# Kernel optimization log

Hardware: AMD Instinct MI355X
Metric: run time of the kernel (lower is better)

## Reference

```python
import jax, jax.numpy as jnp
import numpy as np

DIMS = [1024, 2048, 1024, 1024]


def setup_inputs() -> dict:
    key = jax.random.key(0)
    ks = jax.random.split(key, 13)
    d_in, h1, h2, d_out = DIMS
    s = lambda k, shape, fan_in: jax.random.normal(k, shape, dtype=jnp.float32) / np.sqrt(fan_in)
    return {
        "x": jax.random.normal(ks[0], (4, 2048, d_in), dtype=jnp.float32),
        "w1": s(ks[1], (h1, d_in), d_in), "b1": jnp.zeros((h1,), jnp.float32),
        "w2": s(ks[2], (h2, h1), h1), "b2": jnp.zeros((h2,), jnp.float32),
        "wq": s(ks[3], (h2, h2), h2), "bq": jnp.zeros((h2,), jnp.float32),
        "wk": s(ks[4], (h2, h2), h2), "bk": jnp.zeros((h2,), jnp.float32),
        "wv": s(ks[5], (h2, h2), h2), "bv": jnp.zeros((h2,), jnp.float32),
        "wo": s(ks[6], (d_out, h2), h2), "bo": jnp.zeros((d_out,), jnp.float32),
    }


def reference(x, w1, b1, w2, b2, wq, bq, wk, bk, wv, bv, wo, bo):
    # MLP: Linear + ReLU twice (torch Linear: x @ W^T + b)
    h = jax.nn.relu(jnp.einsum('bsd,hd->bsh', x, w1) + b1)
    h = jax.nn.relu(jnp.einsum('bsh,eh->bse', h, w2) + b2)
    # Self-attention (single head over full hidden_dim)
    q = jnp.einsum('bse,fe->bsf', h, wq) + bq
    k = jnp.einsum('bse,fe->bsf', h, wk) + bk
    v = jnp.einsum('bse,fe->bsf', h, wv) + bv
    hidden_dim = wq.shape[0]
    scores = jnp.einsum('bsf,btf->bst', q, k) / jnp.sqrt(jnp.float32(hidden_dim))
    attn = jax.nn.softmax(scores, axis=-1)
    ctx = jnp.einsum('bst,btf->bsf', attn, v) + v  # residual with V
    return jnp.einsum('bsf,of->bso', ctx, wo) + bo
```

## Files before the change

### kernel.cpp

```cpp
#include <hip/hip_runtime.h>
#include <hip/hip_bf16.h>

typedef __bf16 bf16;
typedef bf16 bf16x8 __attribute__((ext_vector_type(8)));
typedef float f32x4 __attribute__((ext_vector_type(4)));

#define EPI_BIAS_RELU  0
#define EPI_BIAS_BF16  1
#define EPI_PLAIN_BF16 2
#define EPI_RESID      3
#define EPI_BIAS_F32   4

__device__ __forceinline__ void lds_load16(const bf16* g, bf16* l) {
  __builtin_amdgcn_global_load_lds((__attribute__((address_space(1))) void*)g,
                                   (__attribute__((address_space(3))) void*)l,
                                   16, 0, 0);
}

template<int N> __device__ __forceinline__ void vmw() {
  if constexpr (N == 0) asm volatile("s_waitcnt vmcnt(0)" ::: "memory");
  else if constexpr (N == 2) asm volatile("s_waitcnt vmcnt(2)" ::: "memory");
  else if constexpr (N == 4) asm volatile("s_waitcnt vmcnt(4)" ::: "memory");
}
__device__ __forceinline__ void barrier() { asm volatile("s_barrier" ::: "memory"); }

__device__ __forceinline__ void xcd_map(int& bx, int& by, int& z) {
  const int gx = gridDim.x, gy = gridDim.y;
  const int Y8 = (gy * gridDim.z) >> 3;
  const int L = (blockIdx.z * gy + blockIdx.y) * gx + blockIdx.x;
  const int xcd = L & 7, j = L >> 3;
  bx = j % gx;
  const int yy = xcd * Y8 + j / gx;
  by = yy % gy;
  z  = yy / gy;
}

template<int EPI>
__global__ __launch_bounds__(512, 2)
void gemm2x(const bf16* __restrict__ A, const bf16* __restrict__ B,
            void* __restrict__ Cv, const float* __restrict__ bias,
            int K, int lda, int ldb, int ldc,
            long long sAz, long long sBz, long long sCz)
{
  constexpr int BK = 64;
  constexpr int M_REP = 8, N_REP = 4, NH = 2;

  __shared__ __align__(16) bf16 lA[2][256 * BK];
  __shared__ __align__(16) bf16 lB[2][256 * BK];

  int bx, by, z;
  xcd_map(bx, by, z);

  const bf16* Ab = A + (size_t)z * sAz;
  const bf16* Bb = B + (size_t)z * sBz;
  const int row0 = by * 256, col0 = bx * 256;
  const int tid = threadIdx.x, w = tid >> 6, l = tid & 63;
  const int wr = w >> 2, wc = w & 3;

  const int srow = l >> 3, scb = (l & 7) ^ srow;
  const bf16* gA = Ab + (size_t)(row0 + w * 8 + srow) * lda + scb * 8;
  const bf16* gB = Bb + (size_t)(col0 + w * 8 + srow) * ldb + scb * 8;

  auto issueA = [&](int buf, int k0) {
#pragma unroll
    for (int i = 0; i < 4; i++)
      lds_load16(gA + (size_t)(i * 64) * lda + k0,
                 &lA[buf][(i * 64 + w * 8) * BK]);
  };
  auto issueB = [&](int buf, int k0) {
#pragma unroll
    for (int i = 0; i < 4; i++)
      lds_load16(gB + (size_t)(i * 64) * ldb + k0,
                 &lB[buf][(i * 64 + w * 8) * BK]);
  };

  const int fr = l & 15, fq = l >> 4, sw = fr & 7;
  bf16x8 aA[M_REP][2], bB0[NH][2], bB1[NH][2];
  f32x4 acc[M_REP][N_REP] = {};

  auto readAfull = [&](int buf) {
#pragma unroll
    for (int m = 0; m < M_REP; m++) {
      const int r = (m >> 2) * 128 + wr * 64 + (m & 3) * 16 + fr;
      const bf16* base = &lA[buf][r * BK];
#pragma unroll
      for (int kk = 0; kk < 2; kk++)
        aA[m][kk] = *(const bf16x8*)(base + ((kk * 4 + fq) ^ sw) * 8);
    }
  };
  auto readB = [&](bf16x8 (&dst)[NH][2], int buf, int h) {
#pragma unroll
    for (int nn = 0; nn < NH; nn++) {
      const bf16* base = &lB[buf][(h * 128 + wc * 32 + nn * 16 + fr) * BK];
#pragma unroll
      for (int kk = 0; kk < 2; kk++)
        dst[nn][kk] = *(const bf16x8*)(base + ((kk * 4 + fq) ^ sw) * 8);
    }
  };
  auto quad32 = [&](const bf16x8 (&b)[NH][2], int nBase) {
    __builtin_amdgcn_s_setprio(1);
#pragma unroll
    for (int m = 0; m < M_REP; m++)
#pragma unroll
      for (int nh = 0; nh < NH; nh++)
#pragma unroll
        for (int kk = 0; kk < 2; kk++)
          acc[m][nBase + nh] = __builtin_amdgcn_mfma_f32_16x16x32_bf16(
              aA[m][kk], b[nh][kk], acc[m][nBase + nh], 0, 0, 0);
    __builtin_amdgcn_s_setprio(0);
  };

  const int NT = K / BK;
  issueA(0, 0); issueB(0, 0); issueA(1, BK);
  vmw<4>();
  barrier();

  for (int t = 0; t < NT; t++) {
    const int cur = t & 1, nxt = cur ^ 1;
    const bool s1 = (t + 1 < NT), s2 = (t + 2 < NT);
    readAfull(cur);
    readB(bB0, cur, 0);
    if (s1) issueB(nxt, (t + 1) * BK);
    barrier();
    quad32(bB0, 0);
    barrier();
    readB(bB1, cur, 1);
    if (s2) { issueA(cur, (t + 2) * BK); vmw<4>(); }
    else vmw<0>();
    barrier();
    quad32(bB1, NH);
    barrier();
  }

#pragma unroll
  for (int m = 0; m < M_REP; m++) {
#pragma unroll
    for (int n = 0; n < N_REP; n++) {
      const int col = col0 + (n / NH) * 128 + wc * 32 + (n % NH) * 16 + fr;
#pragma unroll
      for (int j = 0; j < 4; j++) {
        const int rrow = row0 + (m >> 2) * 128 + wr * 64 + (m & 3) * 16 + fq * 4 + j;
        const float val = acc[m][n][j];
        if constexpr (EPI == EPI_PLAIN_BF16) {
          bf16* Cp = (bf16*)Cv + (size_t)z * sCz;
          Cp[(size_t)rrow * ldc + col] = (bf16)val;
        } else if constexpr (EPI == EPI_BIAS_BF16) {
          bf16* Cp = (bf16*)Cv;
          Cp[(size_t)rrow * ldc + col] = (bf16)(val + bias[col]);
        } else if constexpr (EPI == EPI_BIAS_RELU) {
          bf16* Cp = (bf16*)Cv;
          Cp[(size_t)rrow * ldc + col] = (bf16)fmaxf(val + bias[col], 0.f);
        }
      }
    }
  }
}

template<int EPI>
__global__ __launch_bounds__(512, 2)
void gemm2p(const bf16* __restrict__ A, const bf16* __restrict__ B,
            void* __restrict__ Cv, const float* __restrict__ bias,
            const bf16* __restrict__ resid,
            int K, int lda, int ldb, int ldc, int ldr,
            long long sAz, long long sBz, long long sCz, long long sRz)
{
  constexpr int BM = 128, BK = 64;
  constexpr int M_REP = 4, NH = 2;

  __shared__ __align__(16) bf16 lA[2][BM * BK];
  __shared__ __align__(16) bf16 lB[2][256 * BK];

  int bx, by, z;
  xcd_map(bx, by, z);

  const bf16* Ab = A + (size_t)z * sAz;
  const bf16* Bb = B + (size_t)z * sBz;
  const int row0 = by * BM, col0 = bx * 256;
  const int tid = threadIdx.x, w = tid >> 6, l = tid & 63;
  const int wr = w >> 2, wc = w & 3;

  const int srow = l >> 3, scb = (l & 7) ^ srow;
  const bf16* gA = Ab + (size_t)(row0 + w * 8 + srow) * lda + scb * 8;
  const bf16* gB = Bb + (size_t)(col0 + w * 8 + srow) * ldb + scb * 8;

  auto issueAfull = [&](int buf, int k0) {
#pragma unroll
    for (int i = 0; i < 2; i++)
      lds_load16(gA + (size_t)(i * 64) * lda + k0,
                 &lA[buf][(i * 64 + w * 8) * BK]);
  };
  auto issueBfull = [&](int buf, int k0) {
#pragma unroll
    for (int i = 0; i < 4; i++)
      lds_load16(gB + (size_t)(i * 64) * ldb + k0,
                 &lB[buf][(i * 64 + w * 8) * BK]);
  };

  const int fr = l & 15, fq = l >> 4, sw = fr & 7;
  bf16x8 aA[M_REP][2], bB0[NH][2], bB1[NH][2];
  f32x4 acc[M_REP][4] = {};

  auto readAfull = [&](int buf) {
#pragma unroll
    for (int m = 0; m < M_REP; m++) {
      const bf16* base = &lA[buf][(wr * 64 + m * 16 + fr) * BK];
#pragma unroll
      for (int kk = 0; kk < 2; kk++)
        aA[m][kk] = *(const bf16x8*)(base + ((kk * 4 + fq) ^ sw) * 8);
    }
  };
  auto readB = [&](bf16x8 (&dst)[NH][2], int buf, int h) {
#pragma unroll
    for (int nn = 0; nn < NH; nn++) {
      const bf16* base = &lB[buf][(h * 128 + wc * 32 + nn * 16 + fr) * BK];
#pragma unroll
      for (int kk = 0; kk < 2; kk++)
        dst[nn][kk] = *(const bf16x8*)(base + ((kk * 4 + fq) ^ sw) * 8);
    }
  };
  auto quad2 = [&](const bf16x8 (&b)[NH][2], int nBase) {
    __builtin_amdgcn_s_setprio(1);
#pragma unroll
    for (int m = 0; m < M_REP; m++)
#pragma unroll
      for (int nh = 0; nh < NH; nh++)
#pragma unroll
        for (int kk = 0; kk < 2; kk++)
          acc[m][nBase + nh] = __builtin_amdgcn_mfma_f32_16x16x32_bf16(
              aA[m][kk], b[nh][kk], acc[m][nBase + nh], 0, 0, 0);
    __builtin_amdgcn_s_setprio(0);
  };

  const int NT = K / BK;
  issueAfull(0, 0); issueBfull(0, 0); issueAfull(1, BK);
  vmw<2>();
  barrier();

  for (int t = 0; t < NT; t++) {
    const int cur = t & 1, nxt = cur ^ 1;
    const bool s1 = (t + 1 < NT), s2 = (t + 2 < NT);
    readAfull(cur);
    readB(bB0, cur, 0);
    if (s1) issueBfull(nxt, (t + 1) * BK);
    barrier();
    quad2(bB0, 0);
    barrier();
    readB(bB1, cur, 1);
    if (s2) { issueAfull(cur, (t + 2) * BK); vmw<2>(); }
    else vmw<0>();
    barrier();
    quad2(bB1, NH);
    barrier();
  }

#pragma unroll
  for (int m = 0; m < M_REP; m++) {
#pragma unroll
    for (int n = 0; n < 4; n++) {
      const int col = col0 + (n / NH) * 128 + wc * 32 + (n % NH) * 16 + fr;
#pragma unroll
      for (int j = 0; j < 4; j++) {
        const int rrow = row0 + wr * 64 + m * 16 + fq * 4 + j;
        const float val = acc[m][n][j];
        if constexpr (EPI == EPI_PLAIN_BF16) {
          bf16* Cp = (bf16*)Cv + (size_t)z * sCz;
          Cp[(size_t)rrow * ldc + col] = (bf16)val;
        } else if constexpr (EPI == EPI_BIAS_F32) {
          float* Cp = (float*)Cv;
          Cp[(size_t)rrow * ldc + col] = val + bias[col];
        } else if constexpr (EPI == EPI_BIAS_BF16) {
          bf16* Cp = (bf16*)Cv;
          Cp[(size_t)rrow * ldc + col] = (bf16)(val + bias[col]);
        } else if constexpr (EPI == EPI_BIAS_RELU) {
          bf16* Cp = (bf16*)Cv;
          Cp[(size_t)rrow * ldc + col] = (bf16)fmaxf(val + bias[col], 0.f);
        } else {
          bf16* Cp = (bf16*)Cv + (size_t)z * sCz;
          const bf16* Rp = resid + (size_t)z * sRz;
          Cp[(size_t)rrow * ldc + col] = (bf16)(val + (float)Rp[(size_t)rrow * ldr + col]);
        }
      }
    }
  }
}

__global__ __launch_bounds__(256)
void cast_all(const float* __restrict__ x,  const float* __restrict__ w1,
              const float* __restrict__ w2, const float* __restrict__ wq,
              const float* __restrict__ wk, const float* __restrict__ wv,
              const float* __restrict__ wo,
              bf16* __restrict__ xb, bf16* __restrict__ w1b,
              bf16* __restrict__ w2b, bf16* __restrict__ wqkb,
              bf16* __restrict__ wvb, bf16* __restrict__ wob) {
  const int b = blockIdx.x;
  const float* src; bf16* dst; int base; float scale = 1.f;
  if (b < 4096)      { src = x;  dst = xb;   base = b; }
  else if (b < 5120) { src = w1; dst = w1b;  base = b - 4096; }
  else if (b < 6144) { src = w2; dst = w2b;  base = b - 5120; }
  else if (b < 6656) { src = wq; dst = wqkb;              base = b - 6144; scale = 0.03125f; }
  else if (b < 7168) { src = wk; dst = wqkb + (1 << 20);  base = b - 6656; }
  else if (b < 7680) { src = wv; dst = wvb;  base = b - 7168; }
  else               { src = wo; dst = wob;  base = b - 7680; }
  const int i = base * 256 + threadIdx.x;
  const float4* p = (const float4*)src;
  float4 a = p[2 * i], c = p[2 * i + 1];
  bf16x8 o8;
  o8[0] = (bf16)(a.x * scale); o8[1] = (bf16)(a.y * scale);
  o8[2] = (bf16)(a.z * scale); o8[3] = (bf16)(a.w * scale);
  o8[4] = (bf16)(c.x * scale); o8[5] = (bf16)(c.y * scale);
  o8[6] = (bf16)(c.z * scale); o8[7] = (bf16)(c.w * scale);
  ((bf16x8*)dst)[i] = o8;
}

__global__ __launch_bounds__(256)
void pack_bias_qk(const float* __restrict__ bq, const float* __restrict__ bk,
                  float* __restrict__ o) {
  int i = blockIdx.x * 256 + threadIdx.x;
  o[i] = (i < 1024) ? bq[i] * 0.03125f : bk[i - 1024];
}

__global__ __launch_bounds__(256)
void transpose_bf16(const bf16* __restrict__ in, bf16* __restrict__ out,
                    int R, int C, int ldi,
                    long long inZ, long long outZ) {
  __shared__ bf16 t[64][72];
  const bf16* ib = in + (size_t)blockIdx.z * inZ;
  bf16* ob = out + (size_t)blockIdx.z * outZ;
  const int r0 = blockIdx.y * 64, c0 = blockIdx.x * 64;
  const int tid = threadIdx.x;
#pragma unroll
  for (int p = 0; p < 2; p++) {
    int r = p * 32 + tid / 8, cc = (tid % 8) * 8;
    bf16x8 vv = *(const bf16x8*)(ib + (size_t)(r0 + r) * ldi + c0 + cc);
#pragma unroll
    for (int j = 0; j < 8; j++) t[r][cc + j] = vv[j];
  }
  __syncthreads();
#pragma unroll
  for (int p = 0; p < 2; p++) {
    int r = p * 32 + tid / 8, cc = (tid % 8) * 8;
    bf16x8 o;
#pragma unroll
    for (int j = 0; j < 8; j++) o[j] = t[cc + j][r];
    *(bf16x8*)(ob + (size_t)(c0 + r) * R + r0 + cc) = o;
  }
}

__global__ __launch_bounds__(256)
void softmax_rows(bf16* __restrict__ S) {
  const size_t row = blockIdx.x;
  const int t = threadIdx.x, wv_ = t >> 6, ln = t & 63;
  bf16x8 v8 = ((const bf16x8*)(S + row * 2048))[t];
  float v[8];
#pragma unroll
  for (int j = 0; j < 8; j++) v[j] = (float)v8[j];
  float m = v[0];
#pragma unroll
  for (int j = 1; j < 8; j++) m = fmaxf(m, v[j]);
  for (int o = 32; o; o >>= 1) m = fmaxf(m, __shfl_xor(m, o));
  __shared__ float redm[4], reds[4];
  if (ln == 0) redm[wv_] = m;
  __syncthreads();
  m = fmaxf(fmaxf(redm[0], redm[1]), fmaxf(redm[2], redm[3]));
  float e[8], s = 0.f;
#pragma unroll
  for (int j = 0; j < 8; j++) { e[j] = __expf(v[j] - m); s += e[j]; }
  for (int o = 32; o; o >>= 1) s += __shfl_xor(s, o);
  if (ln == 0) reds[wv_] = s;
  __syncthreads();
  s = reds[0] + reds[1] + reds[2] + reds[3];
  const float inv = 1.f / s;
  bf16x8 o8;
#pragma unroll
  for (int j = 0; j < 8; j++) o8[j] = (bf16)(e[j] * inv);
  ((bf16x8*)(S + row * 2048))[t] = o8;
}

extern "C" void kernel_launch(void* const* d_in, const int* in_sizes, int n_in,
                              void* d_out, int out_size, void* d_ws, size_t ws_size,
                              hipStream_t stream) {
  const float* x  = (const float*)d_in[0];
  const float* w1 = (const float*)d_in[1];
  const float* b1 = (const float*)d_in[2];
  const float* w2 = (const float*)d_in[3];
  const float* b2 = (const float*)d_in[4];
  const float* wq = (const float*)d_in[5];
  const float* bq = (const float*)d_in[6];
  const float* wk = (const float*)d_in[7];
  const float* bk = (const float*)d_in[8];
  const float* wv = (const float*)d_in[9];
  const float* bv = (const float*)d_in[10];
  const float* wo = (const float*)d_in[11];
  const float* bo = (const float*)d_in[12];
  float* out = (float*)d_out;

  char* ws = (char*)d_ws;
  const size_t MB = 1024ull * 1024ull;
  if (ws_size < 130 * MB) return;

  bf16* w1b  = (bf16*)(ws + 0 * MB);
  bf16* w2b  = (bf16*)(ws + 4 * MB);
  bf16* wqkb = (bf16*)(ws + 8 * MB);
  bf16* wvb  = (bf16*)(ws + 12 * MB);
  bf16* wob  = (bf16*)(ws + 14 * MB);
  float* bqk = (float*)(ws + 16 * MB);
  bf16* xb  = (bf16*)(ws + 17 * MB);
  bf16* h1  = (bf16*)(ws + 33 * MB);
  bf16* h   = (bf16*)(ws + 65 * MB);
  bf16* qk  = (bf16*)(ws + 81 * MB);
  bf16* vb  = (bf16*)(ws + 113 * MB);
  bf16* vT  = (bf16*)(ws + 17 * MB);
  bf16* S   = (bf16*)(ws + 33 * MB);
  bf16* ctx = (bf16*)(ws + 65 * MB);

  cast_all<<<8192, 256, 0, stream>>>(x, w1, w2, wq, wk, wv, wo,
                                     xb, w1b, w2b, wqkb, wvb, wob);
  pack_bias_qk<<<8, 256, 0, stream>>>(bq, bk, bqk);

  gemm2x<EPI_BIAS_RELU><<<dim3(8, 32, 1), 512, 0, stream>>>(
      xb, w1b, h1, b1, 1024, 1024, 1024, 2048, 0, 0, 0);
  gemm2p<EPI_BIAS_RELU><<<dim3(4, 64, 1), 512, 0, stream>>>(
      h1, w2b, h, b2, nullptr, 2048, 2048, 2048, 1024, 0, 0, 0, 0, 0);
  gemm2x<EPI_BIAS_BF16><<<dim3(8, 32, 1), 512, 0, stream>>>(
      h, wqkb, qk, bqk, 1024, 1024, 1024, 2048, 0, 0, 0);
  gemm2p<EPI_BIAS_BF16><<<dim3(4, 64, 1), 512, 0, stream>>>(
      h, wvb, vb, bv, nullptr, 1024, 1024, 1024, 1024, 0, 0, 0, 0, 0);
  transpose_bf16<<<dim3(16, 32, 4), 256, 0, stream>>>(
      vb, vT, 2048, 1024, 1024, 2048LL * 1024, 1024LL * 2048);
  gemm2x<EPI_PLAIN_BF16><<<dim3(8, 8, 4), 512, 0, stream>>>(
      qk, qk + 1024, S, nullptr, 1024, 2048, 2048, 2048,
      2048LL * 2048, 2048LL * 2048, 2048LL * 2048);
  softmax_rows<<<8192, 256, 0, stream>>>(S);
  gemm2p<EPI_RESID><<<dim3(4, 16, 4), 512, 0, stream>>>(
      S, vT, ctx, nullptr, vb, 2048, 2048, 2048, 1024, 1024,
      2048LL * 2048, 1024LL * 2048, 2048LL * 1024, 2048LL * 1024);
  gemm2p<EPI_BIAS_F32><<<dim3(4, 64, 1), 512, 0, stream>>>(
      ctx, wob, out, bo, nullptr, 1024, 1024, 1024, 1024, 0, 0, 0, 0, 0);
}
```

Before: 266.6 us.

## Fuse fp32-to-bf16 cast of x into first GEMM and merge bias packing

Adds a gemm2xa kernel that loads fp32 x directly from global memory into registers, converts it to bf16 and writes it to LDS, so the separate cast pass over x and its bf16 copy in the workspace are no longer needed. The weight cast kernel also absorbs the q/k bias packing, which removes one launch. MFMA loop order in the existing GEMMs is changed to iterate kk outermost. In exchange, the first GEMM reads A at twice the bytes and performs the register-staged conversion inside the main loop, which adds VGPR pressure and manual vmcnt/lgkmcnt waits.

```diff
diff --git a/kernel.cpp b/kernel.cpp
--- a/kernel.cpp
+++ b/kernel.cpp
@@ -21,6 +21,10 @@
   if constexpr (N == 0) asm volatile("s_waitcnt vmcnt(0)" ::: "memory");
   else if constexpr (N == 2) asm volatile("s_waitcnt vmcnt(2)" ::: "memory");
   else if constexpr (N == 4) asm volatile("s_waitcnt vmcnt(4)" ::: "memory");
+  else if constexpr (N == 8) asm volatile("s_waitcnt vmcnt(8)" ::: "memory");
+}
+__device__ __forceinline__ void lgkm0() {
+  asm volatile("s_waitcnt lgkmcnt(0)" ::: "memory");
 }
 __device__ __forceinline__ void barrier() { asm volatile("s_barrier" ::: "memory"); }
 
@@ -100,11 +104,11 @@
   auto quad32 = [&](const bf16x8 (&b)[NH][2], int nBase) {
     __builtin_amdgcn_s_setprio(1);
 #pragma unroll
-    for (int m = 0; m < M_REP; m++)
-#pragma unroll
-      for (int nh = 0; nh < NH; nh++)
-#pragma unroll
-        for (int kk = 0; kk < 2; kk++)
+    for (int kk = 0; kk < 2; kk++)
+#pragma unroll
+      for (int m = 0; m < M_REP; m++)
+#pragma unroll
+        for (int nh = 0; nh < NH; nh++)
           acc[m][nBase + nh] = __builtin_amdgcn_mfma_f32_16x16x32_bf16(
               aA[m][kk], b[nh][kk], acc[m][nBase + nh], 0, 0, 0);
     __builtin_amdgcn_s_setprio(0);
@@ -156,6 +160,140 @@
   }
 }
 
+__global__ __launch_bounds__(512, 2)
+void gemm2xa(const float* __restrict__ Af, const bf16* __restrict__ B,
+             bf16* __restrict__ C, const float* __restrict__ bias,
+             int K, int lda, int ldb, int ldc)
+{
+  constexpr int BK = 64;
+  constexpr int M_REP = 8, N_REP = 4, NH = 2;
+
+  __shared__ __align__(16) bf16 lA[2][256 * BK];
+  __shared__ __align__(16) bf16 lB[2][256 * BK];
+
+  int bx, by, z;
+  xcd_map(bx, by, z);
+
+  const int row0 = by * 256, col0 = bx * 256;
+  const int tid = threadIdx.x, w = tid >> 6, l = tid & 63;
+  const int wr = w >> 2, wc = w & 3;
+
+  const int srow = l >> 3, cb0 = l & 7, scb = cb0 ^ srow;
+  const float* gAf = Af + (size_t)(row0 + w * 8 + srow) * lda + cb0 * 8;
+  const bf16*  gB  = B  + (size_t)(col0 + w * 8 + srow) * ldb + scb * 8;
+
+  float4 aST[4][2];
+
+  auto loadA = [&](int k0) {
+#pragma unroll
+    for (int i = 0; i < 4; i++) {
+      const float* p = gAf + (size_t)(i * 64) * lda + k0;
+      aST[i][0] = *(const float4*)(p);
+      aST[i][1] = *(const float4*)(p + 4);
+    }
+  };
+  auto writeA = [&](int buf) {
+#pragma unroll
+    for (int i = 0; i < 4; i++) {
+      bf16x8 o;
+      o[0] = (bf16)aST[i][0].x; o[1] = (bf16)aST[i][0].y;
+      o[2] = (bf16)aST[i][0].z; o[3] = (bf16)aST[i][0].w;
+      o[4] = (bf16)aST[i][1].x; o[5] = (bf16)aST[i][1].y;
+      o[6] = (bf16)aST[i][1].z; o[7] = (bf16)aST[i][1].w;
+      *(bf16x8*)(&lA[buf][(i * 64 + w * 8 + srow) * BK + scb * 8]) = o;
+    }
+  };
+  auto issueB = [&](int buf, int k0) {
+#pragma unroll
+    for (int i = 0; i < 4; i++)
+      lds_load16(gB + (size_t)(i * 64) * ldb + k0,
+                 &lB[buf][(i * 64 + w * 8) * BK]);
+  };
+
+  const int fr = l & 15, fq = l >> 4, sw = fr & 7;
+  bf16x8 aA[M_REP][2], bB0[NH][2], bB1[NH][2];
+  f32x4 acc[M_REP][N_REP] = {};
+
+  auto readAfull = [&](int buf) {
+#pragma unroll
+    for (int m = 0; m < M_REP; m++) {
+      const int r = (m >> 2) * 128 + wr * 64 + (m & 3) * 16 + fr;
+      const bf16* base = &lA[buf][r * BK];
+#pragma unroll
+      for (int kk = 0; kk < 2; kk++)
+        aA[m][kk] = *(const bf16x8*)(base + ((kk * 4 + fq) ^ sw) * 8);
+    }
+  };
+  auto readB = [&](bf16x8 (&dst)[NH][2], int buf, int h) {
+#pragma unroll
+    for (int nn = 0; nn < NH; nn++) {
+      const bf16* base = &lB[buf][(h * 128 + wc * 32 + nn * 16 + fr) * BK];
+#pragma unroll
+      for (int kk = 0; kk < 2; kk++)
+        dst[nn][kk] = *(const bf16x8*)(base + ((kk * 4 + fq) ^ sw) * 8);
+    }
+  };
+  auto quad32 = [&](const bf16x8 (&b)[NH][2], int nBase) {
+    __builtin_amdgcn_s_setprio(1);
+#pragma unroll
+    for (int kk = 0; kk < 2; kk++)
+#pragma unroll
+      for (int m = 0; m < M_REP; m++)
+#pragma unroll
+        for (int nh = 0; nh < NH; nh++)
+          acc[m][nBase + nh] = __builtin_amdgcn_mfma_f32_16x16x32_bf16(
+              aA[m][kk], b[nh][kk], acc[m][nBase + nh], 0, 0, 0);
+    __builtin_amdgcn_s_setprio(0);
+  };
+
+  const int NT = K / BK;
+  loadA(0);
+  issueB(0, 0);
+  vmw<4>();
+  writeA(0);
+  loadA(BK);
+  vmw<8>();
+  lgkm0();
+  barrier();
+
+  for (int t = 0; t < NT; t++) {
+    const int cur = t & 1, nxt = cur ^ 1;
+    const bool s1 = (t + 1 < NT), s2 = (t + 2 < NT);
+    readAfull(cur);
+    readB(bB0, cur, 0);
+    if (s1) issueB(nxt, (t + 1) * BK);
+    barrier();
+    quad32(bB0, 0);
+    barrier();
+    readB(bB1, cur, 1);
+    if (s1) {
+      vmw<4>();
+      writeA(nxt);
+      if (s2) { loadA((t + 2) * BK); vmw<8>(); }
+      else vmw<0>();
+      lgkm0();
+    } else {
+      vmw<0>();
+    }
+    barrier();
+    quad32(bB1, NH);
+    barrier();
+  }
+
+#pragma unroll
+  for (int m = 0; m < M_REP; m++) {
+#pragma unroll
+    for (int n = 0; n < N_REP; n++) {
+      const int col = col0 + (n / NH) * 128 + wc * 32 + (n % NH) * 16 + fr;
+#pragma unroll
+      for (int j = 0; j < 4; j++) {
+        const int rrow = row0 + (m >> 2) * 128 + wr * 64 + (m & 3) * 16 + fq * 4 + j;
+        C[(size_t)rrow * ldc + col] = (bf16)fmaxf(acc[m][n][j] + bias[col], 0.f);
+      }
+    }
+  }
+}
+
 template<int EPI>
 __global__ __launch_bounds__(512, 2)
 void gemm2p(const bf16* __restrict__ A, const bf16* __restrict__ B,
@@ -221,11 +359,11 @@
   auto quad2 = [&](const bf16x8 (&b)[NH][2], int nBase) {
     __builtin_amdgcn_s_setprio(1);
 #pragma unroll
-    for (int m = 0; m < M_REP; m++)
-#pragma unroll
-      for (int nh = 0; nh < NH; nh++)
-#pragma unroll
-        for (int kk = 0; kk < 2; kk++)
+    for (int kk = 0; kk < 2; kk++)
+#pragma unroll
+      for (int m = 0; m < M_REP; m++)
+#pragma unroll
+        for (int nh = 0; nh < NH; nh++)
           acc[m][nBase + nh] = __builtin_amdgcn_mfma_f32_16x16x32_bf16(
               aA[m][kk], b[nh][kk], acc[m][nBase + nh], 0, 0, 0);
     __builtin_amdgcn_s_setprio(0);
@@ -285,22 +423,26 @@
 }
 
 __global__ __launch_bounds__(256)
-void cast_all(const float* __restrict__ x,  const float* __restrict__ w1,
-              const float* __restrict__ w2, const float* __restrict__ wq,
-              const float* __restrict__ wk, const float* __restrict__ wv,
-              const float* __restrict__ wo,
-              bf16* __restrict__ xb, bf16* __restrict__ w1b,
-              bf16* __restrict__ w2b, bf16* __restrict__ wqkb,
-              bf16* __restrict__ wvb, bf16* __restrict__ wob) {
+void cast_w(const float* __restrict__ w1, const float* __restrict__ w2,
+            const float* __restrict__ wq, const float* __restrict__ wk,
+            const float* __restrict__ wv, const float* __restrict__ wo,
+            const float* __restrict__ bq, const float* __restrict__ bk,
+            bf16* __restrict__ w1b, bf16* __restrict__ w2b,
+            bf16* __restrict__ wqkb, bf16* __restrict__ wvb,
+            bf16* __restrict__ wob, float* __restrict__ bqk) {
   const int b = blockIdx.x;
+  if (b >= 4096) {
+    const int i = (b - 4096) * 256 + threadIdx.x;
+    bqk[i] = (i < 1024) ? bq[i] * 0.03125f : bk[i - 1024];
+    return;
+  }
   const float* src; bf16* dst; int base; float scale = 1.f;
-  if (b < 4096)      { src = x;  dst = xb;   base = b; }
-  else if (b < 5120) { src = w1; dst = w1b;  base = b - 4096; }
-  else if (b < 6144) { src = w2; dst = w2b;  base = b - 5120; }
-  else if (b < 6656) { src = wq; dst = wqkb;              base = b - 6144; scale = 0.03125f; }
-  else if (b < 7168) { src = wk; dst = wqkb + (1 << 20);  base = b - 6656; }
-  else if (b < 7680) { src = wv; dst = wvb;  base = b - 7168; }
-  else               { src = wo; dst = wob;  base = b - 7680; }
+  if (b < 1024)      { src = w1; dst = w1b;  base = b; }
+  else if (b < 2048) { src = w2; dst = w2b;  base = b - 1024; }
+  else if (b < 2560) { src = wq; dst = wqkb;              base = b - 2048; scale = 0.03125f; }
+  else if (b < 3072) { src = wk; dst = wqkb + (1 << 20);  base = b - 2560; }
+  else if (b < 3584) { src = wv; dst = wvb;  base = b - 3072; }
+  else               { src = wo; dst = wob;  base = b - 3584; }
   const int i = base * 256 + threadIdx.x;
   const float4* p = (const float4*)src;
   float4 a = p[2 * i], c = p[2 * i + 1];
@@ -310,13 +452,6 @@
   o8[4] = (bf16)(c.x * scale); o8[5] = (bf16)(c.y * scale);
   o8[6] = (bf16)(c.z * scale); o8[7] = (bf16)(c.w * scale);
   ((bf16x8*)dst)[i] = o8;
-}
-
-__global__ __launch_bounds__(256)
-void pack_bias_qk(const float* __restrict__ bq, const float* __restrict__ bk,
-                  float* __restrict__ o) {
-  int i = blockIdx.x * 256 + threadIdx.x;
-  o[i] = (i < 1024) ? bq[i] * 0.03125f : bk[i - 1024];
 }
 
 __global__ __launch_bounds__(256)
@@ -404,7 +539,6 @@
   bf16* wvb  = (bf16*)(ws + 12 * MB);
   bf16* wob  = (bf16*)(ws + 14 * MB);
   float* bqk = (float*)(ws + 16 * MB);
-  bf16* xb  = (bf16*)(ws + 17 * MB);
   bf16* h1  = (bf16*)(ws + 33 * MB);
   bf16* h   = (bf16*)(ws + 65 * MB);
   bf16* qk  = (bf16*)(ws + 81 * MB);
@@ -413,12 +547,11 @@
   bf16* S   = (bf16*)(ws + 33 * MB);
   bf16* ctx = (bf16*)(ws + 65 * MB);
 
-  cast_all<<<8192, 256, 0, stream>>>(x, w1, w2, wq, wk, wv, wo,
-                                     xb, w1b, w2b, wqkb, wvb, wob);
-  pack_bias_qk<<<8, 256, 0, stream>>>(bq, bk, bqk);
-
-  gemm2x<EPI_BIAS_RELU><<<dim3(8, 32, 1), 512, 0, stream>>>(
-      xb, w1b, h1, b1, 1024, 1024, 1024, 2048, 0, 0, 0);
+  cast_w<<<4104, 256, 0, stream>>>(w1, w2, wq, wk, wv, wo, bq, bk,
+                                   w1b, w2b, wqkb, wvb, wob, bqk);
+
+  gemm2xa<<<dim3(8, 32, 1), 512, 0, stream>>>(
+      x, w1b, h1, b1, 1024, 1024, 1024, 2048);
   gemm2p<EPI_BIAS_RELU><<<dim3(4, 64, 1), 512, 0, stream>>>(
       h1, w2b, h, b2, nullptr, 2048, 2048, 2048, 1024, 0, 0, 0, 0, 0);
   gemm2x<EPI_BIAS_BF16><<<dim3(8, 32, 1), 512, 0, stream>>>(
```

Measured after the change: 296.1 us. 1.11x slower.
